# Optimization experiments

Hardware: AMD Instinct MI355X
Metric: run time of the kernel (lower is better)

Reference implementation:

```python
import jax, jax.numpy as jnp
import numpy as np

ALPHA = 0.2  # LeakyReLU negative slope (module init arg)


def setup_inputs() -> dict:
    key = jax.random.key(0)
    ks = jax.random.split(key, 5)
    b, w, K, E = 8, 256, 256, 512  # batch, window_size, n_features, embed (=2*window)
    x = jax.random.normal(ks[0], (b, w, K), dtype=jnp.float32)
    W = jax.random.normal(ks[1], (E, 2 * w), dtype=jnp.float32) * 0.05
    b_lin = jax.random.normal(ks[2], (E,), dtype=jnp.float32) * 0.05
    a = jax.random.normal(ks[3], (E,), dtype=jnp.float32) * 0.05
    bias = jax.random.normal(ks[4], (K, K), dtype=jnp.float32) * 0.05
    return {"x": x, "W": W, "b_lin": b_lin, "a": a, "bias": bias}


def reference(x, W, b_lin, a, bias):
    # x: (b, window, K) -> v: (b, K, window)
    v = jnp.transpose(x, (0, 2, 1))
    w = v.shape[2]
    # lin(concat(v_i, v_j)) == v_i @ Wl^T + v_j @ Wr^T + b_lin  (split weight)
    Wl, Wr = W[:, :w], W[:, w:]
    left = jnp.einsum('bkw,ew->bke', v, Wl)    # (b, K, E)
    right = jnp.einsum('bkw,ew->bke', v, Wr)   # (b, K, E)
    pre = left[:, :, None, :] + right[:, None, :, :] + b_lin  # (b, K, K, E)
    act = jax.nn.leaky_relu(pre, negative_slope=ALPHA)
    e = jnp.einsum('bije,e->bij', act, a) + bias               # (b, K, K)
    attn = jax.nn.softmax(e, axis=2)  # dropout p=0 in eval -> identity
    h = jax.nn.sigmoid(jnp.einsum('bij,bjw->biw', attn, v))    # (b, K, window)
    return jnp.transpose(h, (0, 2, 1))                          # (b, window, K)
```

## Files before the change

kernel.cpp:

```cpp
#include <hip/hip_runtime.h>
#include <math.h>

typedef float f32x4 __attribute__((ext_vector_type(4)));
typedef __bf16 bf16x8 __attribute__((ext_vector_type(8)));
typedef unsigned short u16x8 __attribute__((ext_vector_type(8)));

__device__ __forceinline__ unsigned short f2bf(float f) {
    union { float f; unsigned int u; } v; v.f = f;
    unsigned int u = v.u;
    return (unsigned short)((u + 0x7fffu + ((u >> 16) & 1u)) >> 16);
}
__device__ __forceinline__ float bf_lo(unsigned int d) {
    union { unsigned int u; float f; } v; v.u = d << 16; return v.f;
}
__device__ __forceinline__ float bf_hi(unsigned int d) {
    union { unsigned int u; float f; } v; v.u = d & 0xffff0000u; return v.f;
}
__device__ __forceinline__ float sigmoidf_(float v) {
    return 1.f / (1.f + __expf(-v));
}

__global__ __launch_bounds__(256) void mfma_gemm_kernel(
    const float* __restrict__ x,
    const float* __restrict__ W,
    const float* __restrict__ b_lin,
    float* __restrict__ LpT,
    unsigned short* __restrict__ R2,
    unsigned short* __restrict__ xbf)
{
    const int b = blockIdx.y;
    const int t = blockIdx.x;

    if (t >= 64) {
        const int idx = b * 65536 + (t - 64) * 2048 + threadIdx.x * 8;
        const float4 v0 = *(const float4*)(x + idx);
        const float4 v1 = *(const float4*)(x + idx + 4);
        u16x8 o;
        o[0] = f2bf(v0.x); o[1] = f2bf(v0.y); o[2] = f2bf(v0.z); o[3] = f2bf(v0.w);
        o[4] = f2bf(v1.x); o[5] = f2bf(v1.y); o[6] = f2bf(v1.z); o[7] = f2bf(v1.w);
        *(u16x8*)(xbf + idx) = o;
        return;
    }

    const bool left = (t < 32);
    int m0, n0;
    if (left) { m0 = (t >> 3) * 64; n0 = (t & 7) * 64; }
    else      { const int tt = t - 32; m0 = (tt >> 2) * 64; n0 = (tt & 3) * 64; }

    __shared__ unsigned short As[64][72];
    __shared__ unsigned short Bs[64][72];

    unsigned short (*Ts)[72] = left ? As : Bs;
    unsigned short (*Ds)[72] = left ? Bs : As;
    const int cbase = left ? m0 : n0;
    const int rbase = left ? n0 : m0;
    const int coff  = left ? 0 : 256;

    const int tid  = threadIdx.x;
    const int wv   = tid >> 6;
    const int lane = tid & 63;
    const int wy = wv >> 1, wx = wv & 1;
    const int lr = lane & 15;
    const int lk = lane >> 4;

    const float* xb = x + b * 65536;

    f32x4 acc[2][2];
    #pragma unroll
    for (int i = 0; i < 2; i++)
        #pragma unroll
        for (int jj = 0; jj < 2; jj++) acc[i][jj] = (f32x4){0.f, 0.f, 0.f, 0.f};

    const int wl = tid >> 4;
    const int kg = tid & 15;
    const int dr = tid >> 2;
    const int dc = (tid & 3) * 16;

    for (int k0 = 0; k0 < 256; k0 += 64) {
        #pragma unroll
        for (int p = 0; p < 4; p++) {
            const int w = wl + 16 * p;
            const float4 v = *(const float4*)(xb + (k0 + w) * 256 + cbase + kg * 4);
            Ts[kg * 4 + 0][w] = f2bf(v.x);
            Ts[kg * 4 + 1][w] = f2bf(v.y);
            Ts[kg * 4 + 2][w] = f2bf(v.z);
            Ts[kg * 4 + 3][w] = f2bf(v.w);
        }
        {
            const float* src = W + (rbase + dr) * 512 + coff + k0 + dc;
            const float4 v0 = *(const float4*)(src);
            const float4 v1 = *(const float4*)(src + 4);
            const float4 v2 = *(const float4*)(src + 8);
            const float4 v3 = *(const float4*)(src + 12);
            u16x8 o0, o1;
            o0[0]=f2bf(v0.x); o0[1]=f2bf(v0.y); o0[2]=f2bf(v0.z); o0[3]=f2bf(v0.w);
            o0[4]=f2bf(v1.x); o0[5]=f2bf(v1.y); o0[6]=f2bf(v1.z); o0[7]=f2bf(v1.w);
            o1[0]=f2bf(v2.x); o1[1]=f2bf(v2.y); o1[2]=f2bf(v2.z); o1[3]=f2bf(v2.w);
            o1[4]=f2bf(v3.x); o1[5]=f2bf(v3.y); o1[6]=f2bf(v3.z); o1[7]=f2bf(v3.w);
            *(u16x8*)&Ds[dr][dc]     = o0;
            *(u16x8*)&Ds[dr][dc + 8] = o1;
        }
        __syncthreads();
        #pragma unroll
        for (int kk = 0; kk < 64; kk += 32) {
            const bf16x8 a0 = *(const bf16x8*)&As[wy * 32 + lr][kk + lk * 8];
            const bf16x8 a1 = *(const bf16x8*)&As[wy * 32 + 16 + lr][kk + lk * 8];
            const bf16x8 b0 = *(const bf16x8*)&Bs[wx * 32 + lr][kk + lk * 8];
            const bf16x8 b1 = *(const bf16x8*)&Bs[wx * 32 + 16 + lr][kk + lk * 8];
            acc[0][0] = __builtin_amdgcn_mfma_f32_16x16x32_bf16(a0, b0, acc[0][0], 0, 0, 0);
            acc[0][1] = __builtin_amdgcn_mfma_f32_16x16x32_bf16(a0, b1, acc[0][1], 0, 0, 0);
            acc[1][0] = __builtin_amdgcn_mfma_f32_16x16x32_bf16(a1, b0, acc[1][0], 0, 0, 0);
            acc[1][1] = __builtin_amdgcn_mfma_f32_16x16x32_bf16(a1, b1, acc[1][1], 0, 0, 0);
        }
        __syncthreads();
    }

    if (left) {
        #pragma unroll
        for (int mi = 0; mi < 2; mi++) {
            #pragma unroll
            for (int ni = 0; ni < 2; ni++) {
                const int row = m0 + wy * 32 + mi * 16 + lk * 4;
                const int col = n0 + wx * 32 + ni * 16 + lr;
                const float bl = b_lin[col];
                float4 o;
                o.x = acc[mi][ni][0] + bl;
                o.y = acc[mi][ni][1] + bl;
                o.z = acc[mi][ni][2] + bl;
                o.w = acc[mi][ni][3] + bl;
                *(float4*)(LpT + b * 131072 + (row >> 2) * 2048 + col * 4) = o;
            }
        }
    } else {
        unsigned short* R2b = R2 + b * 131072;
        #pragma unroll
        for (int mi = 0; mi < 2; mi++) {
            #pragma unroll
            for (int ni = 0; ni < 2; ni++) {
                const int row = m0 + wy * 32 + mi * 16 + lk * 4;
                const int col = n0 + wx * 32 + ni * 16 + lr;
                ushort4 o;
                o.x = f2bf(acc[mi][ni][0]);
                o.y = f2bf(acc[mi][ni][1]);
                o.z = f2bf(acc[mi][ni][2]);
                o.w = f2bf(acc[mi][ni][3]);
                *(ushort4*)(R2b + (row >> 3) * 2048 + col * 8 + (row & 7)) = o;
            }
        }
    }
}

__global__ __launch_bounds__(1024, 8) void attn_kernel(
    const unsigned short* __restrict__ xbf,
    const float* __restrict__ LpT,
    const unsigned int* __restrict__ R2u,
    const float* __restrict__ a,
    const float* __restrict__ bias,
    float* __restrict__ out)
{
    const int b     = blockIdx.x & 7;
    const int itile = blockIdx.x >> 3;
    const int i0    = itile * 4;
    const int tid   = threadIdx.x;
    const int j     = tid & 255;
    const int wv    = tid >> 6;
    const int lane  = tid & 63;

    __shared__ float acc2P[4][4][256];
    __shared__ float rgp[4][256];
    __shared__ float u15p[8][4];
    __shared__ unsigned short atbf[16 * 264];

    const int ehq = __builtin_amdgcn_readfirstlane(tid >> 8);

    const float* Lq = LpT + b * 131072 + itile * 2048 + ehq * 512;
    const float* aq = a + ehq * 128;
    const uint4* Rq = (const uint4*)(R2u + b * 65536) + (ehq * 16) * 256 + j;

    uint4 rb0 = Rq[0];
    uint4 rb1 = Rq[256];

    if (tid < 512) {
        const float4 lv = *(const float4*)(LpT + b * 131072 + itile * 2048 + tid * 4);
        const float ae = a[tid];
        float p0 = ae * lv.x, p1 = ae * lv.y, p2 = ae * lv.z, p3 = ae * lv.w;
        #pragma unroll
        for (int off = 32; off; off >>= 1) {
            p0 += __shfl_xor(p0, off);
            p1 += __shfl_xor(p1, off);
            p2 += __shfl_xor(p2, off);
            p3 += __shfl_xor(p3, off);
        }
        if (lane == 0) {
            u15p[wv][0] = p0; u15p[wv][1] = p1;
            u15p[wv][2] = p2; u15p[wv][3] = p3;
        }
    }

    float acc0 = 0.f, acc1 = 0.f, acc2 = 0.f, acc3 = 0.f, rsum = 0.f;

    #pragma unroll 2
    for (int tk = 0; tk < 16; tk++) {
        uint4 rb2;
        if (tk < 14) rb2 = Rq[(tk + 2) * 256];
        float r[8];
        r[0] = bf_lo(rb0.x); r[1] = bf_hi(rb0.x);
        r[2] = bf_lo(rb0.y); r[3] = bf_hi(rb0.y);
        r[4] = bf_lo(rb0.z); r[5] = bf_hi(rb0.z);
        r[6] = bf_lo(rb0.w); r[7] = bf_hi(rb0.w);
        #pragma unroll
        for (int g = 0; g < 2; g++) {
            const float4 av4 = *(const float4*)(aq + tk * 8 + g * 4);
            const float4 l0 = *(const float4*)(Lq + (tk * 8 + g * 4 + 0) * 4);
            const float4 l1 = *(const float4*)(Lq + (tk * 8 + g * 4 + 1) * 4);
            const float4 l2 = *(const float4*)(Lq + (tk * 8 + g * 4 + 2) * 4);
            const float4 l3 = *(const float4*)(Lq + (tk * 8 + g * 4 + 3) * 4);
            const float rv0 = r[g * 4 + 0];
            const float rv1 = r[g * 4 + 1];
            const float rv2 = r[g * 4 + 2];
            const float rv3 = r[g * 4 + 3];
            rsum = fmaf(av4.x, rv0, rsum);
            acc0 = fmaf(av4.x, fabsf(l0.x + rv0), acc0);
            acc1 = fmaf(av4.x, fabsf(l0.y + rv0), acc1);
            acc2 = fmaf(av4.x, fabsf(l0.z + rv0), acc2);
            acc3 = fmaf(av4.x, fabsf(l0.w + rv0), acc3);
            rsum = fmaf(av4.y, rv1, rsum);
            acc0 = fmaf(av4.y, fabsf(l1.x + rv1), acc0);
            acc1 = fmaf(av4.y, fabsf(l1.y + rv1), acc1);
            acc2 = fmaf(av4.y, fabsf(l1.z + rv1), acc2);
            acc3 = fmaf(av4.y, fabsf(l1.w + rv1), acc3);
            rsum = fmaf(av4.z, rv2, rsum);
            acc0 = fmaf(av4.z, fabsf(l2.x + rv2), acc0);
            acc1 = fmaf(av4.z, fabsf(l2.y + rv2), acc1);
            acc2 = fmaf(av4.z, fabsf(l2.z + rv2), acc2);
            acc3 = fmaf(av4.z, fabsf(l2.w + rv2), acc3);
            rsum = fmaf(av4.w, rv3, rsum);
            acc0 = fmaf(av4.w, fabsf(l3.x + rv3), acc0);
            acc1 = fmaf(av4.w, fabsf(l3.y + rv3), acc1);
            acc2 = fmaf(av4.w, fabsf(l3.z + rv3), acc2);
            acc3 = fmaf(av4.w, fabsf(l3.w + rv3), acc3);
        }
        rb0 = rb1;
        rb1 = rb2;
    }
    acc2P[ehq][0][j] = acc0;
    acc2P[ehq][1][j] = acc1;
    acc2P[ehq][2][j] = acc2;
    acc2P[ehq][3][j] = acc3;
    rgp[ehq][j] = rsum;

    const int lr = lane & 15;
    const int lk = lane >> 4;
    const unsigned short* xw = xbf + b * 65536 + (wv * 16 + lr) * 256;
    const bf16x8 px0 = *(const bf16x8*)(xw + 0 * 32 + lk * 8);
    const bf16x8 px1 = *(const bf16x8*)(xw + 1 * 32 + lk * 8);
    const bf16x8 px2 = *(const bf16x8*)(xw + 2 * 32 + lk * 8);
    const bf16x8 px3 = *(const bf16x8*)(xw + 3 * 32 + lk * 8);

    float bs0 = 0.f, bs1 = 0.f, bs2 = 0.f, bs3 = 0.f;
    if (wv < 4) {
        const float* brow = bias + (i0 + wv) * 256 + lane;
        bs0 = brow[0];
        bs1 = brow[64];
        bs2 = brow[128];
        bs3 = brow[192];
    }
    __syncthreads();

    if (wv < 4) {
        const int i = wv;
        float u15 = 0.f;
        #pragma unroll
        for (int q = 0; q < 8; q++) u15 += u15p[q][i];
        u15 *= 0.6f;
        float v[4];
        const float bsv[4] = { bs0, bs1, bs2, bs3 };
        float m = -1e30f;
        #pragma unroll
        for (int u = 0; u < 4; u++) {
            const int jj = lane + 64 * u;
            const float uR = rgp[0][jj] + rgp[1][jj] + rgp[2][jj] + rgp[3][jj];
            const float ab = acc2P[0][i][jj] + acc2P[1][i][jj]
                           + acc2P[2][i][jj] + acc2P[3][i][jj];
            v[u] = u15 + 0.6f * uR + 0.4f * ab + bsv[u];
            m = fmaxf(m, v[u]);
        }
        #pragma unroll
        for (int off = 32; off; off >>= 1) m = fmaxf(m, __shfl_xor(m, off));
        float ssum = 0.f;
        #pragma unroll
        for (int u = 0; u < 4; u++) { v[u] = __expf(v[u] - m); ssum += v[u]; }
        #pragma unroll
        for (int off = 32; off; off >>= 1) ssum += __shfl_xor(ssum, off);
        const float inv = 1.f / ssum;
        #pragma unroll
        for (int u = 0; u < 4; u++)
            atbf[i * 264 + lane + 64 * u] = f2bf(v[u] * inv);
    }
    __syncthreads();

    {
        f32x4 hacc = (f32x4){0.f, 0.f, 0.f, 0.f};
        const bf16x8 a0 = *(const bf16x8*)&atbf[lr * 264 + 0 * 32 + lk * 8];
        hacc = __builtin_amdgcn_mfma_f32_16x16x32_bf16(a0, px0, hacc, 0, 0, 0);
        const bf16x8 a1 = *(const bf16x8*)&atbf[lr * 264 + 1 * 32 + lk * 8];
        hacc = __builtin_amdgcn_mfma_f32_16x16x32_bf16(a1, px1, hacc, 0, 0, 0);
        const bf16x8 a2 = *(const bf16x8*)&atbf[lr * 264 + 2 * 32 + lk * 8];
        hacc = __builtin_amdgcn_mfma_f32_16x16x32_bf16(a2, px2, hacc, 0, 0, 0);
        const bf16x8 a3 = *(const bf16x8*)&atbf[lr * 264 + 3 * 32 + lk * 8];
        hacc = __builtin_amdgcn_mfma_f32_16x16x32_bf16(a3, px3, hacc, 0, 0, 0);
        #pragma unroll
        for (int kt = 4; kt < 8; kt++) {
            const bf16x8 av = *(const bf16x8*)&atbf[lr * 264 + kt * 32 + lk * 8];
            const bf16x8 bv = *(const bf16x8*)(xw + kt * 32 + lk * 8);
            hacc = __builtin_amdgcn_mfma_f32_16x16x32_bf16(av, bv, hacc, 0, 0, 0);
        }
        if (lk == 0) {
            float4 o;
            o.x = sigmoidf_(hacc[0]);
            o.y = sigmoidf_(hacc[1]);
            o.z = sigmoidf_(hacc[2]);
            o.w = sigmoidf_(hacc[3]);
            *(float4*)(out + b * 65536 + (wv * 16 + lr) * 256 + i0) = o;
        }
    }
}

extern "C" void kernel_launch(void* const* d_in, const int* in_sizes, int n_in,
                              void* d_out, int out_size, void* d_ws, size_t ws_size,
                              hipStream_t stream) {
    const float* x     = (const float*)d_in[0];
    const float* W     = (const float*)d_in[1];
    const float* b_lin = (const float*)d_in[2];
    const float* a     = (const float*)d_in[3];
    const float* bias  = (const float*)d_in[4];
    float* out = (float*)d_out;

    char* ws = (char*)d_ws;
    float*          LpT = (float*)ws;
    unsigned short* R2  = (unsigned short*)(ws + (4 << 20));
    unsigned short* xbf = (unsigned short*)(ws + (6 << 20));

    mfma_gemm_kernel<<<dim3(96, 8), 256, 0, stream>>>(x, W, b_lin, LpT, R2, xbf);
    attn_kernel<<<512, 1024, 0, stream>>>(xbf, LpT, (const unsigned int*)R2,
                                          a, bias, out);
}
```

Baseline: 98.70 us.

## Fuse left/right projections per tile and precompute a·R row sums in GEMM

The GEMM kernel now computes both the left and right projections in one block, sharing the transposed x tile, which halves the GEMM block count and the x staging. It also computes the per-column dot of a with the right projection in the epilogue and accumulates it with atomics into a small buffer. This removes the rsum accumulation from the attention kernel's hot loop and the shared-memory reduction that went with it. The cost is an extra memset launch, float atomics whose summation order varies between runs, and more register and shared-memory use per GEMM block.

```diff
diff --git a/kernel.cpp b/kernel.cpp
--- a/kernel.cpp
+++ b/kernel.cpp
@@ -24,15 +24,17 @@
     const float* __restrict__ x,
     const float* __restrict__ W,
     const float* __restrict__ b_lin,
+    const float* __restrict__ a,
     float* __restrict__ LpT,
     unsigned short* __restrict__ R2,
-    unsigned short* __restrict__ xbf)
+    unsigned short* __restrict__ xbf,
+    float* __restrict__ uRb)
 {
     const int b = blockIdx.y;
     const int t = blockIdx.x;
 
-    if (t >= 64) {
-        const int idx = b * 65536 + (t - 64) * 2048 + threadIdx.x * 8;
+    if (t >= 32) {
+        const int idx = b * 65536 + (t - 32) * 2048 + threadIdx.x * 8;
         const float4 v0 = *(const float4*)(x + idx);
         const float4 v1 = *(const float4*)(x + idx + 4);
         u16x8 o;
@@ -42,19 +44,14 @@
         return;
     }
 
-    const bool left = (t < 32);
-    int m0, n0;
-    if (left) { m0 = (t >> 3) * 64; n0 = (t & 7) * 64; }
-    else      { const int tt = t - 32; m0 = (tt >> 2) * 64; n0 = (tt & 3) * 64; }
-
-    __shared__ unsigned short As[64][72];
-    __shared__ unsigned short Bs[64][72];
-
-    unsigned short (*Ts)[72] = left ? As : Bs;
-    unsigned short (*Ds)[72] = left ? Bs : As;
-    const int cbase = left ? m0 : n0;
-    const int rbase = left ? n0 : m0;
-    const int coff  = left ? 0 : 256;
+    const int c  = t & 3;
+    const int e  = t >> 2;
+    const int c0 = c * 64;
+    const int e0 = e * 64;
+
+    __shared__ unsigned short Ts[64][72];
+    __shared__ unsigned short Dl[64][72];
+    __shared__ unsigned short Dr[64][72];
 
     const int tid  = threadIdx.x;
     const int wv   = tid >> 6;
@@ -65,11 +62,14 @@
 
     const float* xb = x + b * 65536;
 
-    f32x4 acc[2][2];
+    f32x4 accl[2][2], accr[2][2];
     #pragma unroll
     for (int i = 0; i < 2; i++)
         #pragma unroll
-        for (int jj = 0; jj < 2; jj++) acc[i][jj] = (f32x4){0.f, 0.f, 0.f, 0.f};
+        for (int jj = 0; jj < 2; jj++) {
+            accl[i][jj] = (f32x4){0.f, 0.f, 0.f, 0.f};
+            accr[i][jj] = (f32x4){0.f, 0.f, 0.f, 0.f};
+        }
 
     const int wl = tid >> 4;
     const int kg = tid & 15;
@@ -80,73 +80,100 @@
         #pragma unroll
         for (int p = 0; p < 4; p++) {
             const int w = wl + 16 * p;
-            const float4 v = *(const float4*)(xb + (k0 + w) * 256 + cbase + kg * 4);
+            const float4 v = *(const float4*)(xb + (k0 + w) * 256 + c0 + kg * 4);
             Ts[kg * 4 + 0][w] = f2bf(v.x);
             Ts[kg * 4 + 1][w] = f2bf(v.y);
             Ts[kg * 4 + 2][w] = f2bf(v.z);
             Ts[kg * 4 + 3][w] = f2bf(v.w);
         }
         {
-            const float* src = W + (rbase + dr) * 512 + coff + k0 + dc;
-            const float4 v0 = *(const float4*)(src);
-            const float4 v1 = *(const float4*)(src + 4);
-            const float4 v2 = *(const float4*)(src + 8);
-            const float4 v3 = *(const float4*)(src + 12);
+            const float* srcl = W + (e0 + dr) * 512 + k0 + dc;
+            const float4 v0 = *(const float4*)(srcl);
+            const float4 v1 = *(const float4*)(srcl + 4);
+            const float4 v2 = *(const float4*)(srcl + 8);
+            const float4 v3 = *(const float4*)(srcl + 12);
             u16x8 o0, o1;
             o0[0]=f2bf(v0.x); o0[1]=f2bf(v0.y); o0[2]=f2bf(v0.z); o0[3]=f2bf(v0.w);
             o0[4]=f2bf(v1.x); o0[5]=f2bf(v1.y); o0[6]=f2bf(v1.z); o0[7]=f2bf(v1.w);
             o1[0]=f2bf(v2.x); o1[1]=f2bf(v2.y); o1[2]=f2bf(v2.z); o1[3]=f2bf(v2.w);
             o1[4]=f2bf(v3.x); o1[5]=f2bf(v3.y); o1[6]=f2bf(v3.z); o1[7]=f2bf(v3.w);
-            *(u16x8*)&Ds[dr][dc]     = o0;
-            *(u16x8*)&Ds[dr][dc + 8] = o1;
+            *(u16x8*)&Dl[dr][dc]     = o0;
+            *(u16x8*)&Dl[dr][dc + 8] = o1;
+            const float* srcr = srcl + 256;
+            const float4 w0 = *(const float4*)(srcr);
+            const float4 w1 = *(const float4*)(srcr + 4);
+            const float4 w2 = *(const float4*)(srcr + 8);
+            const float4 w3 = *(const float4*)(srcr + 12);
+            u16x8 q0, q1;
+            q0[0]=f2bf(w0.x); q0[1]=f2bf(w0.y); q0[2]=f2bf(w0.z); q0[3]=f2bf(w0.w);
+            q0[4]=f2bf(w1.x); q0[5]=f2bf(w1.y); q0[6]=f2bf(w1.z); q0[7]=f2bf(w1.w);
+            q1[0]=f2bf(w2.x); q1[1]=f2bf(w2.y); q1[2]=f2bf(w2.z); q1[3]=f2bf(w2.w);
+            q1[4]=f2bf(w3.x); q1[5]=f2bf(w3.y); q1[6]=f2bf(w3.z); q1[7]=f2bf(w3.w);
+            *(u16x8*)&Dr[dr][dc]     = q0;
+            *(u16x8*)&Dr[dr][dc + 8] = q1;
         }
         __syncthreads();
         #pragma unroll
         for (int kk = 0; kk < 64; kk += 32) {
-            const bf16x8 a0 = *(const bf16x8*)&As[wy * 32 + lr][kk + lk * 8];
-            const bf16x8 a1 = *(const bf16x8*)&As[wy * 32 + 16 + lr][kk + lk * 8];
-            const bf16x8 b0 = *(const bf16x8*)&Bs[wx * 32 + lr][kk + lk * 8];
-            const bf16x8 b1 = *(const bf16x8*)&Bs[wx * 32 + 16 + lr][kk + lk * 8];
-            acc[0][0] = __builtin_amdgcn_mfma_f32_16x16x32_bf16(a0, b0, acc[0][0], 0, 0, 0);
-            acc[0][1] = __builtin_amdgcn_mfma_f32_16x16x32_bf16(a0, b1, acc[0][1], 0, 0, 0);
-            acc[1][0] = __builtin_amdgcn_mfma_f32_16x16x32_bf16(a1, b0, acc[1][0], 0, 0, 0);
-            acc[1][1] = __builtin_amdgcn_mfma_f32_16x16x32_bf16(a1, b1, acc[1][1], 0, 0, 0);
+            const bf16x8 t0 = *(const bf16x8*)&Ts[wy * 32 + lr][kk + lk * 8];
+            const bf16x8 t1 = *(const bf16x8*)&Ts[wy * 32 + 16 + lr][kk + lk * 8];
+            const bf16x8 l0 = *(const bf16x8*)&Dl[wx * 32 + lr][kk + lk * 8];
+            const bf16x8 l1 = *(const bf16x8*)&Dl[wx * 32 + 16 + lr][kk + lk * 8];
+            accl[0][0] = __builtin_amdgcn_mfma_f32_16x16x32_bf16(t0, l0, accl[0][0], 0, 0, 0);
+            accl[0][1] = __builtin_amdgcn_mfma_f32_16x16x32_bf16(t0, l1, accl[0][1], 0, 0, 0);
+            accl[1][0] = __builtin_amdgcn_mfma_f32_16x16x32_bf16(t1, l0, accl[1][0], 0, 0, 0);
+            accl[1][1] = __builtin_amdgcn_mfma_f32_16x16x32_bf16(t1, l1, accl[1][1], 0, 0, 0);
+            const bf16x8 r0 = *(const bf16x8*)&Dr[wy * 32 + lr][kk + lk * 8];
+            const bf16x8 r1 = *(const bf16x8*)&Dr[wy * 32 + 16 + lr][kk + lk * 8];
+            const bf16x8 s0 = *(const bf16x8*)&Ts[wx * 32 + lr][kk + lk * 8];
+            const bf16x8 s1 = *(const bf16x8*)&Ts[wx * 32 + 16 + lr][kk + lk * 8];
+            accr[0][0] = __builtin_amdgcn_mfma_f32_16x16x32_bf16(r0, s0, accr[0][0], 0, 0, 0);
+            accr[0][1] = __builtin_amdgcn_mfma_f32_16x16x32_bf16(r0, s1, accr[0][1], 0, 0, 0);
+            accr[1][0] = __builtin_amdgcn_mfma_f32_16x16x32_bf16(r1, s0, accr[1][0], 0, 0, 0);
+            accr[1][1] = __builtin_amdgcn_mfma_f32_16x16x32_bf16(r1, s1, accr[1][1], 0, 0, 0);
         }
         __syncthreads();
     }
 
-    if (left) {
-        #pragma unroll
-        for (int mi = 0; mi < 2; mi++) {
+    #pragma unroll
+    for (int mi = 0; mi < 2; mi++) {
+        #pragma unroll
+        for (int ni = 0; ni < 2; ni++) {
+            const int row = c0 + wy * 32 + mi * 16 + lk * 4;
+            const int col = e0 + wx * 32 + ni * 16 + lr;
+            const float bl = b_lin[col];
+            float4 o;
+            o.x = accl[mi][ni][0] + bl;
+            o.y = accl[mi][ni][1] + bl;
+            o.z = accl[mi][ni][2] + bl;
+            o.w = accl[mi][ni][3] + bl;
+            *(float4*)(LpT + b * 131072 + (row >> 2) * 2048 + col * 4) = o;
+        }
+    }
+    {
+        unsigned short* R2b = R2 + b * 131072;
+        float pj[2] = {0.f, 0.f};
+        int colj[2];
+        #pragma unroll
+        for (int ni = 0; ni < 2; ni++) {
+            colj[ni] = c0 + wx * 32 + ni * 16 + lr;
             #pragma unroll
-            for (int ni = 0; ni < 2; ni++) {
-                const int row = m0 + wy * 32 + mi * 16 + lk * 4;
-                const int col = n0 + wx * 32 + ni * 16 + lr;
-                const float bl = b_lin[col];
-                float4 o;
-                o.x = acc[mi][ni][0] + bl;
-                o.y = acc[mi][ni][1] + bl;
-                o.z = acc[mi][ni][2] + bl;
-                o.w = acc[mi][ni][3] + bl;
-                *(float4*)(LpT + b * 131072 + (row >> 2) * 2048 + col * 4) = o;
+            for (int mi = 0; mi < 2; mi++) {
+                const int row = e0 + wy * 32 + mi * 16 + lk * 4;
+                ushort4 o;
+                o.x = f2bf(accr[mi][ni][0]);
+                o.y = f2bf(accr[mi][ni][1]);
+                o.z = f2bf(accr[mi][ni][2]);
+                o.w = f2bf(accr[mi][ni][3]);
+                *(ushort4*)(R2b + (row >> 3) * 2048 + colj[ni] * 8 + (row & 7)) = o;
+                pj[ni] += a[row + 0] * accr[mi][ni][0]
+                        + a[row + 1] * accr[mi][ni][1]
+                        + a[row + 2] * accr[mi][ni][2]
+                        + a[row + 3] * accr[mi][ni][3];
             }
         }
-    } else {
-        unsigned short* R2b = R2 + b * 131072;
-        #pragma unroll
-        for (int mi = 0; mi < 2; mi++) {
-            #pragma unroll
-            for (int ni = 0; ni < 2; ni++) {
-                const int row = m0 + wy * 32 + mi * 16 + lk * 4;
-                const int col = n0 + wx * 32 + ni * 16 + lr;
-                ushort4 o;
-                o.x = f2bf(acc[mi][ni][0]);
-                o.y = f2bf(acc[mi][ni][1]);
-                o.z = f2bf(acc[mi][ni][2]);
-                o.w = f2bf(acc[mi][ni][3]);
-                *(ushort4*)(R2b + (row >> 3) * 2048 + col * 8 + (row & 7)) = o;
-            }
-        }
+        atomicAdd(&uRb[b * 256 + colj[0]], pj[0]);
+        atomicAdd(&uRb[b * 256 + colj[1]], pj[1]);
     }
 }
 
@@ -156,6 +183,7 @@
     const unsigned int* __restrict__ R2u,
     const float* __restrict__ a,
     const float* __restrict__ bias,
+    const float* __restrict__ uRb,
     float* __restrict__ out)
 {
     const int b     = blockIdx.x & 7;
@@ -167,7 +195,6 @@
     const int lane  = tid & 63;
 
     __shared__ float acc2P[4][4][256];
-    __shared__ float rgp[4][256];
     __shared__ float u15p[8][4];
     __shared__ unsigned short atbf[16 * 264];
 
@@ -197,7 +224,7 @@
         }
     }
 
-    float acc0 = 0.f, acc1 = 0.f, acc2 = 0.f, acc3 = 0.f, rsum = 0.f;
+    float acc0 = 0.f, acc1 = 0.f, acc2 = 0.f, acc3 = 0.f;
 
     #pragma unroll 2
     for (int tk = 0; tk < 16; tk++) {
@@ -219,22 +246,18 @@
             const float rv1 = r[g * 4 + 1];
             const float rv2 = r[g * 4 + 2];
             const float rv3 = r[g * 4 + 3];
-            rsum = fmaf(av4.x, rv0, rsum);
             acc0 = fmaf(av4.x, fabsf(l0.x + rv0), acc0);
             acc1 = fmaf(av4.x, fabsf(l0.y + rv0), acc1);
             acc2 = fmaf(av4.x, fabsf(l0.z + rv0), acc2);
             acc3 = fmaf(av4.x, fabsf(l0.w + rv0), acc3);
-            rsum = fmaf(av4.y, rv1, rsum);
             acc0 = fmaf(av4.y, fabsf(l1.x + rv1), acc0);
             acc1 = fmaf(av4.y, fabsf(l1.y + rv1), acc1);
             acc2 = fmaf(av4.y, fabsf(l1.z + rv1), acc2);
             acc3 = fmaf(av4.y, fabsf(l1.w + rv1), acc3);
-            rsum = fmaf(av4.z, rv2, rsum);
             acc0 = fmaf(av4.z, fabsf(l2.x + rv2), acc0);
             acc1 = fmaf(av4.z, fabsf(l2.y + rv2), acc1);
             acc2 = fmaf(av4.z, fabsf(l2.z + rv2), acc2);
             acc3 = fmaf(av4.z, fabsf(l2.w + rv2), acc3);
-            rsum = fmaf(av4.w, rv3, rsum);
             acc0 = fmaf(av4.w, fabsf(l3.x + rv3), acc0);
             acc1 = fmaf(av4.w, fabsf(l3.y + rv3), acc1);
             acc2 = fmaf(av4.w, fabsf(l3.z + rv3), acc2);
@@ -247,7 +270,6 @@
     acc2P[ehq][1][j] = acc1;
     acc2P[ehq][2][j] = acc2;
     acc2P[ehq][3][j] = acc3;
-    rgp[ehq][j] = rsum;
 
     const int lr = lane & 15;
     const int lk = lane >> 4;
@@ -258,12 +280,18 @@
     const bf16x8 px3 = *(const bf16x8*)(xw + 3 * 32 + lk * 8);
 
     float bs0 = 0.f, bs1 = 0.f, bs2 = 0.f, bs3 = 0.f;
+    float ur0 = 0.f, ur1 = 0.f, ur2 = 0.f, ur3 = 0.f;
     if (wv < 4) {
         const float* brow = bias + (i0 + wv) * 256 + lane;
         bs0 = brow[0];
         bs1 = brow[64];
         bs2 = brow[128];
         bs3 = brow[192];
+        const float* urow = uRb + b * 256 + lane;
+        ur0 = urow[0];
+        ur1 = urow[64];
+        ur2 = urow[128];
+        ur3 = urow[192];
     }
     __syncthreads();
 
@@ -275,14 +303,14 @@
         u15 *= 0.6f;
         float v[4];
         const float bsv[4] = { bs0, bs1, bs2, bs3 };
+        const float urv[4] = { ur0, ur1, ur2, ur3 };
         float m = -1e30f;
         #pragma unroll
         for (int u = 0; u < 4; u++) {
             const int jj = lane + 64 * u;
-            const float uR = rgp[0][jj] + rgp[1][jj] + rgp[2][jj] + rgp[3][jj];
             const float ab = acc2P[0][i][jj] + acc2P[1][i][jj]
                            + acc2P[2][i][jj] + acc2P[3][i][jj];
-            v[u] = u15 + 0.6f * uR + 0.4f * ab + bsv[u];
+            v[u] = u15 + 0.6f * urv[u] + 0.4f * ab + bsv[u];
             m = fmaxf(m, v[u]);
         }
         #pragma unroll
@@ -340,8 +368,11 @@
     float*          LpT = (float*)ws;
     unsigned short* R2  = (unsigned short*)(ws + (4 << 20));
     unsigned short* xbf = (unsigned short*)(ws + (6 << 20));
-
-    mfma_gemm_kernel<<<dim3(96, 8), 256, 0, stream>>>(x, W, b_lin, LpT, R2, xbf);
+    float*          uRb = (float*)(ws + (7 << 20));
+
+    hipMemsetAsync(uRb, 0, 8 * 256 * sizeof(float), stream);
+    mfma_gemm_kernel<<<dim3(64, 8), 256, 0, stream>>>(x, W, b_lin, a,
+                                                      LpT, R2, xbf, uRb);
     attn_kernel<<<512, 1024, 0, stream>>>(xbf, LpT, (const unsigned int*)R2,
-                                          a, bias, out);
-}
+                                          a, bias, uRb, out);
+}
```

Result: slower. 109.8 us (+11.2%).
